# Optimization experiments

Hardware: AMD Instinct MI355X
Metric: run time of the kernel (lower is better)

## Reference

```python
import jax, jax.numpy as jnp
import numpy as np

B = 65536
N_FEATURES = 256   # n_layers = 8
N_PHYS = 2
N_LABELS = 2
BOND = 8


def _layer_shapes():
    # returns list of (n_tensors, d_in, d_out) for layers 7..1, plus root (8,8,2)
    n_layers = int(np.log2(N_FEATURES))
    shapes = []
    # leaf layer l = n_layers-1
    shapes.append((2 ** (n_layers - 1), N_PHYS, min(N_PHYS ** 2, BOND)))
    # intermediate layers l = n_layers-2 .. 1
    for l in range(n_layers - 2, 0, -1):
        d_in = min(N_PHYS ** (n_layers - l), BOND)
        d_out = min(N_PHYS ** (n_layers - l + 1), BOND)
        shapes.append((2 ** l, d_in, d_out))
    return shapes


def setup_inputs() -> dict:
    key = jax.random.key(0)
    keys = jax.random.split(key, 10)
    x = jax.random.normal(keys[0], (B, N_FEATURES, N_PHYS), dtype=jnp.float32)
    inp = {"x": x}
    # stacked per-layer tree tensors, scaled 1/d_in to keep activations O(1)
    names = ["w7", "w6", "w5", "w4", "w3", "w2", "w1"]
    for k, (name, (n_t, d_in, d_out)) in enumerate(zip(names, _layer_shapes())):
        w = jax.random.normal(keys[k + 1], (n_t, d_in, d_in, d_out), dtype=jnp.float32)
        inp[name] = w / d_in
    d_root = min(N_PHYS ** int(np.log2(N_FEATURES)), BOND)
    inp["w0"] = jax.random.normal(keys[9], (d_root, d_root, N_LABELS), dtype=jnp.float32) / d_root
    return inp


def reference(x, w7, w6, w5, w4, w3, w2, w1, w0):
    b = x.shape[0]
    # leaf layer: pair adjacent physical sites -> [B, 128, 4]
    xp = x.reshape(b, N_FEATURES // 2, 2, N_PHYS)
    h = jnp.einsum('bni,bnj,nijk->bnk', xp[:, :, 0], xp[:, :, 1], w7)
    # climb the tree: each level halves the node count
    for w in (w6, w5, w4, w3, w2, w1):
        n = w.shape[0]
        hp = h.reshape(b, n, 2, h.shape[-1])
        h = jnp.einsum('bni,bnj,nijk->bnk', hp[:, :, 0], hp[:, :, 1], w)
    # root: [B, 2, d] -> [B, n_labels]
    out = jnp.einsum('bi,bj,ijl->bl', h[:, 0], h[:, 1], w0)
    return out
```

## Files before the change

kernel.cpp:

```cpp
#include <hip/hip_runtime.h>


__device__ __forceinline__ void combine8(const float* __restrict__ w,
                                         const float L[8], const float R[8],
                                         float out[8]) {
    float acc[8];
#pragma unroll
    for (int k = 0; k < 8; ++k) acc[k] = 0.f;
#pragma unroll
    for (int i = 0; i < 8; ++i) {
#pragma unroll
        for (int j = 0; j < 8; ++j) {
            const float o = L[i] * R[j];
            const float* wp = w + (i * 8 + j) * 8;
#pragma unroll
            for (int k = 0; k < 8; ++k) acc[k] = fmaf(o, wp[k], acc[k]);
        }
    }
#pragma unroll
    for (int k = 0; k < 8; ++k) out[k] = acc[k];
}

__device__ __forceinline__ void copy8(float dst[8], const float src[8]) {
#pragma unroll
    for (int k = 0; k < 8; ++k) dst[k] = src[k];
}

__global__ __launch_bounds__(256, 4)
void tn_tree_kernel(const float* __restrict__ x,
                    const float* __restrict__ w7,
                    const float* __restrict__ w6,
                    const float* __restrict__ w5,
                    const float* __restrict__ w4,
                    const float* __restrict__ w3,
                    const float* __restrict__ w2,
                    const float* __restrict__ w1,
                    const float* __restrict__ w0,
                    float* __restrict__ out) {
    const int lane = threadIdx.x & 63;
    const int q = __builtin_amdgcn_readfirstlane((int)(threadIdx.x >> 6));
    const int b = blockIdx.x * 64 + lane;

    const float* xp = x + (size_t)b * 512 + (size_t)q * 128;

    float p7[4], p6[8], p5[8], p4[8], p3[8], res[8];

#pragma unroll 2
    for (int m = 0; m < 32; ++m) {
        const float4 xv = *reinterpret_cast<const float4*>(xp + m * 4);
        float v4[4];
        {
            const float* w = w7 + (size_t)(32 * q + m) * 16;
            const float o00 = xv.x * xv.z, o01 = xv.x * xv.w;
            const float o10 = xv.y * xv.z, o11 = xv.y * xv.w;
#pragma unroll
            for (int k = 0; k < 4; ++k)
                v4[k] = fmaf(o00, w[k],
                        fmaf(o01, w[4 + k],
                        fmaf(o10, w[8 + k], o11 * w[12 + k])));
        }
        if ((m & 1) == 0) {
#pragma unroll
            for (int k = 0; k < 4; ++k) p7[k] = v4[k];
            continue;
        }

        float v8[8];
        {
            const float* w = w6 + (size_t)(16 * q + (m >> 1)) * 128;
#pragma unroll
            for (int k = 0; k < 8; ++k) v8[k] = 0.f;
#pragma unroll
            for (int i = 0; i < 4; ++i) {
#pragma unroll
                for (int j = 0; j < 4; ++j) {
                    const float o = p7[i] * v4[j];
                    const float* wp = w + (i * 4 + j) * 8;
#pragma unroll
                    for (int k = 0; k < 8; ++k) v8[k] = fmaf(o, wp[k], v8[k]);
                }
            }
        }
        if ((m & 2) == 0) { copy8(p6, v8); continue; }

        float t[8];
        combine8(w5 + (size_t)(8 * q + (m >> 2)) * 512, p6, v8, t);
        if ((m & 4) == 0) { copy8(p5, t); continue; }

        combine8(w4 + (size_t)(4 * q + (m >> 3)) * 512, p5, t, v8);
        if ((m & 8) == 0) { copy8(p4, v8); continue; }

        combine8(w3 + (size_t)(2 * q + (m >> 4)) * 512, p4, v8, t);
        if ((m & 16) == 0) { copy8(p3, t); continue; }

        combine8(w2 + (size_t)q * 512, p3, t, res);
    }

    __shared__ float lds[256][9];
    const int slot = q * 64 + lane;
#pragma unroll
    for (int k = 0; k < 8; ++k) lds[slot][k] = res[k];
    __syncthreads();

    if (q < 2) {
        float L[8], R[8], v1[8];
#pragma unroll
        for (int k = 0; k < 8; ++k) {
            L[k] = lds[2 * q * 64 + lane][k];
            R[k] = lds[(2 * q + 1) * 64 + lane][k];
        }
        combine8(w1 + (size_t)q * 512, L, R, v1);
#pragma unroll
        for (int k = 0; k < 8; ++k) lds[slot][k] = v1[k];
    }
    __syncthreads();

    if (q == 0) {
        float L[8], R[8];
#pragma unroll
        for (int k = 0; k < 8; ++k) {
            L[k] = lds[lane][k];
            R[k] = lds[64 + lane][k];
        }
        float o0 = 0.f, o1 = 0.f;
#pragma unroll
        for (int i = 0; i < 8; ++i) {
#pragma unroll
            for (int j = 0; j < 8; ++j) {
                const float o = L[i] * R[j];
                o0 = fmaf(o, w0[i * 16 + j * 2 + 0], o0);
                o1 = fmaf(o, w0[i * 16 + j * 2 + 1], o1);
            }
        }
        float2 r;
        r.x = o0;
        r.y = o1;
        *reinterpret_cast<float2*>(out + (size_t)b * 2) = r;
    }
}

extern "C" void kernel_launch(void* const* d_in, const int* in_sizes, int n_in,
                              void* d_out, int out_size, void* d_ws, size_t ws_size,
                              hipStream_t stream) {
    const float* x  = (const float*)d_in[0];
    const float* w7 = (const float*)d_in[1];
    const float* w6 = (const float*)d_in[2];
    const float* w5 = (const float*)d_in[3];
    const float* w4 = (const float*)d_in[4];
    const float* w3 = (const float*)d_in[5];
    const float* w2 = (const float*)d_in[6];
    const float* w1 = (const float*)d_in[7];
    const float* w0 = (const float*)d_in[8];
    float* out = (float*)d_out;

    dim3 grid(65536 / 64);
    dim3 block(256);
    hipLaunchKernelGGL(tn_tree_kernel, grid, block, 0, stream,
                       x, w7, w6, w5, w4, w3, w2, w1, w0, out);
}
```

Measured before the change: 283.0 us.

## Split each sample's subtree across eight wavefronts instead of four

Each block now uses 512 threads, so each of eight wavefronts handles a 64-feature subtree for the same 64 samples, up to layer 3. Layer 2 is then combined through LDS by four waves, followed by the existing layer-1 and root steps. This doubles the parallelism per sample and shortens each wave's serial chain, aimed at better latency hiding. In exchange it adds an extra barrier and LDS stage with more idle waves, and launch bounds of 512x8 may tighten register limits.

```diff
diff --git a/kernel.cpp b/kernel.cpp
--- a/kernel.cpp
+++ b/kernel.cpp
@@ -26,7 +26,7 @@
     for (int k = 0; k < 8; ++k) dst[k] = src[k];
 }
 
-__global__ __launch_bounds__(256, 4)
+__global__ __launch_bounds__(512, 8)
 void tn_tree_kernel(const float* __restrict__ x,
                     const float* __restrict__ w7,
                     const float* __restrict__ w6,
@@ -38,19 +38,19 @@
                     const float* __restrict__ w0,
                     float* __restrict__ out) {
     const int lane = threadIdx.x & 63;
-    const int q = __builtin_amdgcn_readfirstlane((int)(threadIdx.x >> 6));
+    const int e = __builtin_amdgcn_readfirstlane((int)(threadIdx.x >> 6));
     const int b = blockIdx.x * 64 + lane;
 
-    const float* xp = x + (size_t)b * 512 + (size_t)q * 128;
+    const float* xp = x + (size_t)b * 512 + (size_t)e * 64;
 
-    float p7[4], p6[8], p5[8], p4[8], p3[8], res[8];
+    float p7[4], p6[8], p5[8], p4[8], res[8];
 
 #pragma unroll 2
-    for (int m = 0; m < 32; ++m) {
+    for (int m = 0; m < 16; ++m) {
         const float4 xv = *reinterpret_cast<const float4*>(xp + m * 4);
         float v4[4];
         {
-            const float* w = w7 + (size_t)(32 * q + m) * 16;
+            const float* w = w7 + (size_t)(16 * e + m) * 16;
             const float o00 = xv.x * xv.z, o01 = xv.x * xv.w;
             const float o10 = xv.y * xv.z, o11 = xv.y * xv.w;
 #pragma unroll
@@ -67,7 +67,7 @@
 
         float v8[8];
         {
-            const float* w = w6 + (size_t)(16 * q + (m >> 1)) * 128;
+            const float* w = w6 + (size_t)(8 * e + (m >> 1)) * 128;
 #pragma unroll
             for (int k = 0; k < 8; ++k) v8[k] = 0.f;
 #pragma unroll
@@ -84,38 +84,48 @@
         if ((m & 2) == 0) { copy8(p6, v8); continue; }
 
         float t[8];
-        combine8(w5 + (size_t)(8 * q + (m >> 2)) * 512, p6, v8, t);
+        combine8(w5 + (size_t)(4 * e + (m >> 2)) * 512, p6, v8, t);
         if ((m & 4) == 0) { copy8(p5, t); continue; }
 
-        combine8(w4 + (size_t)(4 * q + (m >> 3)) * 512, p5, t, v8);
+        combine8(w4 + (size_t)(2 * e + (m >> 3)) * 512, p5, t, v8);
         if ((m & 8) == 0) { copy8(p4, v8); continue; }
 
-        combine8(w3 + (size_t)(2 * q + (m >> 4)) * 512, p4, v8, t);
-        if ((m & 16) == 0) { copy8(p3, t); continue; }
-
-        combine8(w2 + (size_t)q * 512, p3, t, res);
+        combine8(w3 + (size_t)e * 512, p4, v8, res);
     }
 
-    __shared__ float lds[256][9];
-    const int slot = q * 64 + lane;
+    __shared__ float lds[512][9];
+    const int slot = e * 64 + lane;
 #pragma unroll
     for (int k = 0; k < 8; ++k) lds[slot][k] = res[k];
     __syncthreads();
 
-    if (q < 2) {
+    if (e < 4) {
+        float L[8], R[8], v2[8];
+#pragma unroll
+        for (int k = 0; k < 8; ++k) {
+            L[k] = lds[2 * e * 64 + lane][k];
+            R[k] = lds[(2 * e + 1) * 64 + lane][k];
+        }
+        combine8(w2 + (size_t)e * 512, L, R, v2);
+#pragma unroll
+        for (int k = 0; k < 8; ++k) lds[slot][k] = v2[k];
+    }
+    __syncthreads();
+
+    if (e < 2) {
         float L[8], R[8], v1[8];
 #pragma unroll
         for (int k = 0; k < 8; ++k) {
-            L[k] = lds[2 * q * 64 + lane][k];
-            R[k] = lds[(2 * q + 1) * 64 + lane][k];
+            L[k] = lds[2 * e * 64 + lane][k];
+            R[k] = lds[(2 * e + 1) * 64 + lane][k];
         }
-        combine8(w1 + (size_t)q * 512, L, R, v1);
+        combine8(w1 + (size_t)e * 512, L, R, v1);
 #pragma unroll
         for (int k = 0; k < 8; ++k) lds[slot][k] = v1[k];
     }
     __syncthreads();
 
-    if (q == 0) {
+    if (e == 0) {
         float L[8], R[8];
 #pragma unroll
         for (int k = 0; k < 8; ++k) {
@@ -154,7 +164,7 @@
     float* out = (float*)d_out;
 
     dim3 grid(65536 / 64);
-    dim3 block(256);
+    dim3 block(512);
     hipLaunchKernelGGL(tn_tree_kernel, grid, block, 0, stream,
                        x, w7, w6, w5, w4, w3, w2, w1, w0, out);
 }
```

Result: faster. 264.8 us (-6.4%).
